# Kernel optimization log

Hardware: AMD Instinct MI355X
Metric: run time of the kernel (lower is better)

The kernel has to match this reference:

```python
import jax, jax.numpy as jnp
import numpy as np

B, C_IN, C_OUT, H, W = 32, 256, 256, 32, 32


def setup_inputs() -> dict:
    key = jax.random.key(0)
    kx, kw, kb = jax.random.split(key, 3)
    x = jax.random.normal(kx, (B, C_IN, H, W), dtype=jnp.float32)
    # 1x1 conv == pointwise linear over channels: weight [out_c, in_c], bias [out_c]
    conv_w = jax.random.normal(kw, (C_OUT, C_IN), dtype=jnp.float32) * (1.0 / np.sqrt(C_IN))
    conv_b = jax.random.normal(kb, (C_OUT,), dtype=jnp.float32) * 0.01
    return {"x": x, "conv_w": conv_w, "conv_b": conv_b}


def reference(x, conv_w, conv_b):
    b, c, h, w = x.shape
    hw = h * w
    q = x.reshape(b, c, hw)  # q == k == flattened x
    # score[b,i,j] = sum_c q[b,c,i] * q[b,c,j]  -> (b, hw, hw)
    score = jnp.einsum('bci,bcj->bij', q, q)
    attn = jax.nn.softmax(score, axis=-1)
    # 1x1 conv V projection: (b, out_c, h, w)
    v = jnp.einsum('oc,bchw->bohw', conv_w, x) + conv_b[None, :, None, None]
    v = v.reshape(b, -1, hw).transpose(0, 2, 1)  # (b, hw, out_c)
    out = jnp.einsum('bij,bjo->bio', attn, v)  # (b, hw, out_c)
    # torch does .transpose(-1,-1) (a no-op) then reshape(b,-1,h,w) in row-major
    out = out.reshape(b, -1, h, w)  # (b, out_c, h, w), position-major flatten as in torch
    # MaxPool2d(2): 2x2 windows, stride 2
    oc = out.shape[1]
    out = out.reshape(b, oc, h // 2, 2, w // 2, 2).max(axis=(3, 5))
    return out
```

## Files before the change

### kernel.cpp

```cpp
#include <hip/hip_runtime.h>
#include <math.h>

#define BB 32
#define CC 256
#define NN 1024
#define THR 8.0f

typedef unsigned short u16;
typedef unsigned int u32;
typedef u16 u16x8 __attribute__((ext_vector_type(8)));
typedef _Float16 h16;
typedef h16 h16x2 __attribute__((ext_vector_type(2)));
typedef h16 h16x8 __attribute__((ext_vector_type(8)));
typedef float f32x4 __attribute__((ext_vector_type(4)));
typedef float f32x16 __attribute__((ext_vector_type(16)));
typedef u32 u32x4v __attribute__((ext_vector_type(4)));

__device__ __forceinline__ h16x8 ldh8(const u16* p) {
    return __builtin_bit_cast(h16x8, *(const u16x8*)p);
}
__device__ __forceinline__ f32x4 mfma16(h16x8 a, h16x8 b, f32x4 c) {
    return __builtin_amdgcn_mfma_f32_16x16x32_f16(a, b, c, 0, 0, 0);
}
__device__ __forceinline__ f32x16 mfma32(h16x8 a, h16x8 b, f32x16 c) {
    return __builtin_amdgcn_mfma_f32_32x32x16_f16(a, b, c, 0, 0, 0);
}
__device__ __forceinline__ void gll16(const void* g, void* l) {
    __builtin_amdgcn_global_load_lds((const __attribute__((address_space(1))) u32*)g,
                                     (__attribute__((address_space(3))) u32*)l, 16, 0, 0);
}

__global__ __launch_bounds__(256) void k_split(const float* __restrict__ x,
                                               u16* __restrict__ qf,
                                               const float* __restrict__ w,
                                               u16* __restrict__ whf) {
    __shared__ float lds[64][65];
    int bid = blockIdx.x;
    int t = threadIdx.x;
    if (bid >= 2048) {
        int s = (bid - 2048) * 256 + t;
        int ot = s >> 9, ks = (s >> 6) & 7, l = s & 63;
        const float* src = w + (size_t)(ot * 16 + (l & 15)) * CC + ks * 32 + 8 * (l >> 4);
        float4 a = *(const float4*)src;
        float4 c = *(const float4*)(src + 4);
        u16x8 o;
        o[0] = __builtin_bit_cast(u16, (h16)a.x); o[1] = __builtin_bit_cast(u16, (h16)a.y);
        o[2] = __builtin_bit_cast(u16, (h16)a.z); o[3] = __builtin_bit_cast(u16, (h16)a.w);
        o[4] = __builtin_bit_cast(u16, (h16)c.x); o[5] = __builtin_bit_cast(u16, (h16)c.y);
        o[6] = __builtin_bit_cast(u16, (h16)c.z); o[7] = __builtin_bit_cast(u16, (h16)c.w);
        *(u16x8*)(whf + (size_t)s * 8) = o;
        return;
    }
    int b = bid >> 6, ct = (bid >> 4) & 3, pt = bid & 15;
    int c0 = ct * 64, p0 = pt * 64;
    const float* xb = x + ((size_t)b * CC + c0) * NN + p0;
#pragma unroll
    for (int it = 0; it < 4; ++it) {
        int cl = (t >> 4) + it * 16;
        int pl = (t & 15) * 4;
        float4 v = *(const float4*)(xb + (size_t)cl * NN + pl);
        lds[pl + 0][cl] = v.x;
        lds[pl + 1][cl] = v.y;
        lds[pl + 2][cl] = v.z;
        lds[pl + 3][cl] = v.w;
    }
    __syncthreads();
    u16* qb = qf + ((size_t)b * NN + p0) * CC + c0;
#pragma unroll
    for (int it = 0; it < 2; ++it) {
        int pl = (t >> 3) + it * 32;
        int cl = (t & 7) * 8;
        u16x8 hv;
#pragma unroll
        for (int e = 0; e < 8; ++e) hv[e] = __builtin_bit_cast(u16, (h16)lds[pl][cl + e]);
        *(u16x8*)(qb + (size_t)pl * CC + cl) = hv;
    }
}

__global__ __launch_bounds__(256, 4) void k_vgemm(const u16* __restrict__ qf,
                                                  const u16* __restrict__ whf,
                                                  const float* __restrict__ bias,
                                                  u16* __restrict__ vimg) {
    __shared__ __align__(16) u16 smem[10240];
    int bid = blockIdx.x;
    int b = bid >> 5, pt = bid & 31;
    int t = threadIdx.x, wave = t >> 6, lane = t & 63;
    int l15 = lane & 15, l4 = lane >> 4;
    int p0 = pt * 32, o0 = wave * 64;
    {
        int Gb = wave * 256;
#pragma unroll
        for (int inst = 0; inst < 4; ++inst) {
            int G = Gb + inst * 64 + lane;
            int row = G >> 5, g = G & 31;
            gll16(qf + (size_t)(b * NN + p0 + row) * CC + ((g ^ (row & 7)) << 3),
                  smem + (size_t)(Gb + inst * 64) * 8);
        }
    }
    __syncthreads();
    f32x4 acc[4][2];
#pragma unroll
    for (int m = 0; m < 4; ++m)
#pragma unroll
        for (int n = 0; n < 2; ++n) acc[m][n] = (f32x4){0.f, 0.f, 0.f, 0.f};
#pragma unroll
    for (int ks = 0; ks < 8; ++ks) {
        h16x8 afr[4], bfr[2];
#pragma unroll
        for (int m = 0; m < 4; ++m)
            afr[m] = ldh8(whf + (size_t)(((wave * 4 + m) * 8 + ks) * 64 + lane) * 8);
#pragma unroll
        for (int n = 0; n < 2; ++n) {
            int row = n * 16 + l15;
            bfr[n] = ldh8(smem + row * 256 + (((4 * ks + l4) ^ (l15 & 7)) << 3));
        }
#pragma unroll
        for (int m = 0; m < 4; ++m)
#pragma unroll
            for (int n = 0; n < 2; ++n) acc[m][n] = mfma16(afr[m], bfr[n], acc[m][n]);
    }
    __syncthreads();
    u16* Vs = smem + wave * 2560;
#pragma unroll
    for (int m = 0; m < 4; ++m) {
#pragma unroll
        for (int r = 0; r < 4; ++r) {
            int ol = m * 16 + 4 * l4 + r;
            float bv = bias[o0 + ol];
#pragma unroll
            for (int n = 0; n < 2; ++n)
                Vs[ol * 40 + n * 16 + l15] =
                    __builtin_bit_cast(u16, (h16)(acc[m][n][r] + bv));
        }
    }
#pragma unroll
    for (int m = 0; m < 4; ++m) {
        u16x8 v = *(u16x8*)&Vs[(m * 16 + l15) * 40 + 8 * l4];
        *(u16x8*)(vimg + ((size_t)(b * 32 + pt) * 256 + o0 + m * 16 + l15) * 32 + 8 * l4) = v;
    }
}

#define SMEM_A 66560
__global__ __launch_bounds__(256, 2) void k_attn(const u16* __restrict__ qf,
                                                 const u16* __restrict__ vimg,
                                                 float* __restrict__ out) {
    __shared__ __align__(16) char smem[SMEM_A];
    u16* Kb = (u16*)smem;
    u16* Vb = (u16*)(smem + 32768);
    float* Mx = (float*)(smem + 65536);
    float* Lx = (float*)(smem + 66048);
    float* Ob = (float*)smem;

    int bid = blockIdx.x;
    int xcd = bid & 7, s0 = bid >> 3;
    int b = xcd * 4 + (s0 >> 4);
    int i0 = (s0 & 15) * 64;
    int t = threadIdx.x, wave = t >> 6, lane = t & 63;
    int rg = wave & 1, jg = wave >> 1;
    int l31 = lane & 31, lh = lane >> 5, l7 = lane & 7;
    const u16* qb = qf + (size_t)b * NN * CC;
    const u16* vtb = vimg + (size_t)b * (32 * 8192);

    {
        int Gb = wave * 512;
#pragma unroll
        for (int inst = 0; inst < 8; ++inst) {
            int G = Gb + inst * 64 + lane;
            int row = (G >> 5) & 31, g = G & 31, tile = G >> 10;
            gll16(qb + (size_t)(i0 + tile * 32 + row) * CC + ((g ^ (row & 7)) << 3),
                  Kb + (size_t)(Gb + inst * 64) * 8);
        }
    }
    __syncthreads();
    h16x8 qfr[16];
    {
        const u16* qB = Kb + rg * 8192 + l31 * 256;
#pragma unroll
        for (int ks = 0; ks < 16; ++ks)
            qfr[ks] = ldh8(qB + (((2 * ks + lh) ^ l7) << 3));
    }
    __syncthreads();
    {
        int Gb = wave * 512;
#pragma unroll
        for (int inst = 0; inst < 8; ++inst) {
            int G = Gb + inst * 64 + lane;
            int row = (G >> 5) & 31, g = G & 31, tile = G >> 10;
            gll16(qb + (size_t)((tile * 16) * 32 + row) * CC + ((g ^ (row & 7)) << 3),
                  Kb + (size_t)(Gb + inst * 64) * 8);
        }
#pragma unroll
        for (int inst = 0; inst < 8; ++inst) {
            int G = Gb + inst * 64 + lane;
            int row = (G >> 2) & 255, gi = G & 3, tile = G >> 10;
            gll16(vtb + (size_t)(tile * 16) * 8192 + row * 32 + ((gi ^ ((row >> 1) & 3)) << 3),
                  Vb + (size_t)(Gb + inst * 64) * 8);
        }
    }
    __syncthreads();

    f32x16 oacc[8];
#pragma unroll
    for (int oc = 0; oc < 8; ++oc)
#pragma unroll
        for (int r = 0; r < 16; ++r) oacc[oc][r] = 0.f;
    float m = -INFINITY, l = 0.f;
    const u16* KbJ = Kb + jg * 8192;
    const u16* VbJ = Vb + jg * 8192;
    int l31s = (l31 >> 1) & 3;

    for (int it = 0; it < 16; ++it) {
        f32x16 s;
#pragma unroll
        for (int r = 0; r < 16; ++r) s[r] = 0.f;
        __builtin_amdgcn_s_setprio(1);
#pragma unroll
        for (int ks = 0; ks < 16; ++ks) {
            h16x8 a = ldh8(KbJ + l31 * 256 + (((2 * ks + lh) ^ l7) << 3));
            s = mfma32(a, qfr[ks], s);
        }
        __builtin_amdgcn_s_setprio(0);
        __syncthreads();
        if (it < 15) {
            int Gb = wave * 512;
#pragma unroll
            for (int inst = 0; inst < 8; ++inst) {
                int G = Gb + inst * 64 + lane;
                int row = (G >> 5) & 31, g = G & 31, tile = G >> 10;
                gll16(qb + (size_t)((tile * 16 + it + 1) * 32 + row) * CC +
                          ((g ^ (row & 7)) << 3),
                      Kb + (size_t)(Gb + inst * 64) * 8);
            }
        }
        float mx = s[0];
#pragma unroll
        for (int r = 1; r < 16; ++r) mx = fmaxf(mx, s[r]);
        mx = fmaxf(mx, __shfl_xor(mx, 32));
        if (__any(mx > m + THR)) {
            float mn = fmaxf(m, mx);
            float f = __expf(m - mn);
            m = mn;
            l *= f;
#pragma unroll
            for (int oc = 0; oc < 8; ++oc)
#pragma unroll
                for (int r = 0; r < 16; ++r) oacc[oc][r] *= f;
        }
        float p[16], rs = 0.f;
#pragma unroll
        for (int r = 0; r < 16; ++r) { p[r] = __expf(s[r] - m); rs += p[r]; }
        rs += __shfl_xor(rs, 32);
        l += rs;
        u32 pk0 = __builtin_bit_cast(u32, __builtin_amdgcn_cvt_pkrtz(p[0], p[1]));
        u32 pk1 = __builtin_bit_cast(u32, __builtin_amdgcn_cvt_pkrtz(p[2], p[3]));
        u32 pk2 = __builtin_bit_cast(u32, __builtin_amdgcn_cvt_pkrtz(p[4], p[5]));
        u32 pk3 = __builtin_bit_cast(u32, __builtin_amdgcn_cvt_pkrtz(p[6], p[7]));
        u32 pk4 = __builtin_bit_cast(u32, __builtin_amdgcn_cvt_pkrtz(p[8], p[9]));
        u32 pk5 = __builtin_bit_cast(u32, __builtin_amdgcn_cvt_pkrtz(p[10], p[11]));
        u32 pk6 = __builtin_bit_cast(u32, __builtin_amdgcn_cvt_pkrtz(p[12], p[13]));
        u32 pk7 = __builtin_bit_cast(u32, __builtin_amdgcn_cvt_pkrtz(p[14], p[15]));
        asm volatile("v_permlane32_swap_b32 %0, %1" : "+v"(pk0), "+v"(pk2));
        asm volatile("v_permlane32_swap_b32 %0, %1" : "+v"(pk1), "+v"(pk3));
        asm volatile("v_permlane32_swap_b32 %0, %1" : "+v"(pk4), "+v"(pk6));
        asm volatile("v_permlane32_swap_b32 %0, %1" : "+v"(pk5), "+v"(pk7));
        h16x8 pa0 = __builtin_bit_cast(h16x8, (u32x4v){pk0, pk1, pk2, pk3});
        h16x8 pa1 = __builtin_bit_cast(h16x8, (u32x4v){pk4, pk5, pk6, pk7});
        __builtin_amdgcn_s_setprio(1);
#pragma unroll
        for (int oc = 0; oc < 8; ++oc) {
            h16x8 v0 = ldh8(VbJ + (oc * 32 + l31) * 32 + (((0 + lh) ^ l31s) << 3));
            h16x8 v1 = ldh8(VbJ + (oc * 32 + l31) * 32 + (((2 + lh) ^ l31s) << 3));
            oacc[oc] = mfma32(v0, pa0, oacc[oc]);
            oacc[oc] = mfma32(v1, pa1, oacc[oc]);
        }
        __builtin_amdgcn_s_setprio(0);
        __syncthreads();
        if (it < 15) {
            int Gb = wave * 512;
#pragma unroll
            for (int inst = 0; inst < 8; ++inst) {
                int G = Gb + inst * 64 + lane;
                int row = (G >> 2) & 255, gi = G & 3, tile = G >> 10;
                gll16(vtb + (size_t)(tile * 16 + it + 1) * 8192 + row * 32 +
                          ((gi ^ ((row >> 1) & 3)) << 3),
                      Vb + (size_t)(Gb + inst * 64) * 8);
            }
        }
    }

    if (lane < 32) {
        Mx[wave * 32 + l31] = m;
        Lx[wave * 32 + l31] = l;
    }
    if (jg == 1) {
#pragma unroll
        for (int oc = 0; oc < 8; ++oc)
#pragma unroll
            for (int q = 0; q < 4; ++q) {
                f32x4 v = (f32x4){oacc[oc][4 * q + 0], oacc[oc][4 * q + 1],
                                  oacc[oc][4 * q + 2], oacc[oc][4 * q + 3]};
                *(f32x4*)&Ob[(((rg * 8 + oc) * 4 + q) * 64 + lane) * 4] = v;
            }
    }
    __syncthreads();
    if (jg == 0) {
        int pidx = (wave ^ 2) * 32 + l31;
        float m2 = Mx[pidx], l2 = Lx[pidx];
        float ms = fmaxf(m, m2);
        float f0 = __expf(m - ms), f1 = __expf(m2 - ms);
        float inv = 1.f / (l * f0 + l2 * f1);
        f0 *= inv; f1 *= inv;
#pragma unroll
        for (int oc = 0; oc < 8; ++oc)
#pragma unroll
            for (int q = 0; q < 4; ++q) {
                f32x4 o1 = *(const f32x4*)&Ob[(((rg * 8 + oc) * 4 + q) * 64 + lane) * 4];
#pragma unroll
                for (int e = 0; e < 4; ++e)
                    oacc[oc][4 * q + e] = oacc[oc][4 * q + e] * f0 + o1[e] * f1;
            }
        int I = i0 + rg * 32 + l31;
        float* ob = out + ((size_t)(b * 256 + (I >> 2)) * 16 + (I & 3) * 4) * 16;
#pragma unroll
        for (int pl = 0; pl < 4; ++pl) {
#pragma unroll
            for (int pwh = 0; pwh < 8; ++pwh) {
                int r0 = 2 * (pwh & 1) + 4 * (pwh >> 1);
                int oc0 = 2 * pl;
                float v = fmaxf(fmaxf(oacc[oc0][r0], oacc[oc0][r0 + 1]),
                                fmaxf(oacc[oc0 + 1][r0], oacc[oc0 + 1][r0 + 1]));
                int pw = (pwh & 1) + 4 * (pwh >> 1) + 2 * lh;
                ob[pl * 16 + pw] = v;
            }
        }
    }
}

extern "C" void kernel_launch(void* const* d_in, const int* in_sizes, int n_in,
                              void* d_out, int out_size, void* d_ws, size_t ws_size,
                              hipStream_t stream) {
    const float* x = (const float*)d_in[0];
    const float* w = (const float*)d_in[1];
    const float* bias = (const float*)d_in[2];
    float* out = (float*)d_out;
    u16* qf = (u16*)d_ws;
    u16* vimg = qf + (size_t)BB * NN * CC;
    u16* whf = vimg + (size_t)BB * NN * CC;
    k_split<<<2080, 256, 0, stream>>>(x, qf, w, whf);
    k_vgemm<<<1024, 256, 0, stream>>>(qf, whf, bias, vimg);
    k_attn<<<512, 256, 0, stream>>>(qf, vimg, out);
}
```

Before: 172.9 us.

## Fuse x conversion into V-GEMM and store K/V in MFMA fragment order

Merges the fp32-to-fp16 transpose pass into the V projection kernel, which now converts x through LDS and writes both K and V straight into MFMA fragment layouts. The attention kernel then loads Q fragments directly from global memory, double-buffers only K in LDS, and streams V fragments from global into registers without staging. The max-pool output is gathered in LDS so stores are coalesced. This removes one full pass over x and the swizzled LDS staging, at the cost of uncached global V loads inside the inner loop.

```diff
diff --git a/kernel.cpp b/kernel.cpp
--- a/kernel.cpp
+++ b/kernel.cpp
@@ -10,7 +10,6 @@
 typedef unsigned int u32;
 typedef u16 u16x8 __attribute__((ext_vector_type(8)));
 typedef _Float16 h16;
-typedef h16 h16x2 __attribute__((ext_vector_type(2)));
 typedef h16 h16x8 __attribute__((ext_vector_type(8)));
 typedef float f32x4 __attribute__((ext_vector_type(4)));
 typedef float f32x16 __attribute__((ext_vector_type(16)));
@@ -25,131 +24,120 @@
 __device__ __forceinline__ f32x16 mfma32(h16x8 a, h16x8 b, f32x16 c) {
     return __builtin_amdgcn_mfma_f32_32x32x16_f16(a, b, c, 0, 0, 0);
 }
+__device__ __forceinline__ u32 pkrtz(float a, float b) {
+    return __builtin_bit_cast(u32, __builtin_amdgcn_cvt_pkrtz(a, b));
+}
 __device__ __forceinline__ void gll16(const void* g, void* l) {
     __builtin_amdgcn_global_load_lds((const __attribute__((address_space(1))) u32*)g,
                                      (__attribute__((address_space(3))) u32*)l, 16, 0, 0);
 }
 
-__global__ __launch_bounds__(256) void k_split(const float* __restrict__ x,
-                                               u16* __restrict__ qf,
-                                               const float* __restrict__ w,
+__global__ __launch_bounds__(256) void k_wprep(const float* __restrict__ w,
                                                u16* __restrict__ whf) {
-    __shared__ float lds[64][65];
-    int bid = blockIdx.x;
-    int t = threadIdx.x;
-    if (bid >= 2048) {
-        int s = (bid - 2048) * 256 + t;
-        int ot = s >> 9, ks = (s >> 6) & 7, l = s & 63;
-        const float* src = w + (size_t)(ot * 16 + (l & 15)) * CC + ks * 32 + 8 * (l >> 4);
-        float4 a = *(const float4*)src;
-        float4 c = *(const float4*)(src + 4);
-        u16x8 o;
-        o[0] = __builtin_bit_cast(u16, (h16)a.x); o[1] = __builtin_bit_cast(u16, (h16)a.y);
-        o[2] = __builtin_bit_cast(u16, (h16)a.z); o[3] = __builtin_bit_cast(u16, (h16)a.w);
-        o[4] = __builtin_bit_cast(u16, (h16)c.x); o[5] = __builtin_bit_cast(u16, (h16)c.y);
-        o[6] = __builtin_bit_cast(u16, (h16)c.z); o[7] = __builtin_bit_cast(u16, (h16)c.w);
-        *(u16x8*)(whf + (size_t)s * 8) = o;
-        return;
-    }
-    int b = bid >> 6, ct = (bid >> 4) & 3, pt = bid & 15;
-    int c0 = ct * 64, p0 = pt * 64;
-    const float* xb = x + ((size_t)b * CC + c0) * NN + p0;
-#pragma unroll
-    for (int it = 0; it < 4; ++it) {
-        int cl = (t >> 4) + it * 16;
-        int pl = (t & 15) * 4;
-        float4 v = *(const float4*)(xb + (size_t)cl * NN + pl);
-        lds[pl + 0][cl] = v.x;
-        lds[pl + 1][cl] = v.y;
-        lds[pl + 2][cl] = v.z;
-        lds[pl + 3][cl] = v.w;
-    }
-    __syncthreads();
-    u16* qb = qf + ((size_t)b * NN + p0) * CC + c0;
-#pragma unroll
-    for (int it = 0; it < 2; ++it) {
-        int pl = (t >> 3) + it * 32;
-        int cl = (t & 7) * 8;
-        u16x8 hv;
-#pragma unroll
-        for (int e = 0; e < 8; ++e) hv[e] = __builtin_bit_cast(u16, (h16)lds[pl][cl + e]);
-        *(u16x8*)(qb + (size_t)pl * CC + cl) = hv;
-    }
-}
-
-__global__ __launch_bounds__(256, 4) void k_vgemm(const u16* __restrict__ qf,
+    int s = blockIdx.x * 256 + threadIdx.x;
+    int ot = s >> 9, ks = (s >> 6) & 7, l = s & 63;
+    const float* src = w + (size_t)(ot * 16 + (l & 15)) * CC + ks * 32 + 8 * (l >> 4);
+    float4 a = *(const float4*)src;
+    float4 c = *(const float4*)(src + 4);
+    u32x4v o = (u32x4v){pkrtz(a.x, a.y), pkrtz(a.z, a.w), pkrtz(c.x, c.y), pkrtz(c.z, c.w)};
+    *(u32x4v*)(whf + (size_t)s * 8) = o;
+}
+
+__global__ __launch_bounds__(256, 4) void k_xform(const float* __restrict__ x,
                                                   const u16* __restrict__ whf,
                                                   const float* __restrict__ bias,
-                                                  u16* __restrict__ vimg) {
-    __shared__ __align__(16) u16 smem[10240];
+                                                  u16* __restrict__ kf,
+                                                  u16* __restrict__ vf) {
+    __shared__ __align__(16) float xs[32][68];
+    __shared__ __align__(16) u16 Vs[4][64 * 40];
     int bid = blockIdx.x;
     int b = bid >> 5, pt = bid & 31;
     int t = threadIdx.x, wave = t >> 6, lane = t & 63;
-    int l15 = lane & 15, l4 = lane >> 4;
-    int p0 = pt * 32, o0 = wave * 64;
-    {
-        int Gb = wave * 256;
-#pragma unroll
-        for (int inst = 0; inst < 4; ++inst) {
-            int G = Gb + inst * 64 + lane;
-            int row = G >> 5, g = G & 31;
-            gll16(qf + (size_t)(b * NN + p0 + row) * CC + ((g ^ (row & 7)) << 3),
-                  smem + (size_t)(Gb + inst * 64) * 8);
-        }
-    }
-    __syncthreads();
+    int l15 = lane & 15, l4 = lane >> 4, l31 = lane & 31, lh = lane >> 5;
+    int p0 = pt * 32;
+    int r0 = t >> 3, pq = (t & 7) * 4;
+
     f32x4 acc[4][2];
 #pragma unroll
     for (int m = 0; m < 4; ++m)
 #pragma unroll
         for (int n = 0; n < 2; ++n) acc[m][n] = (f32x4){0.f, 0.f, 0.f, 0.f};
-#pragma unroll
-    for (int ks = 0; ks < 8; ++ks) {
-        h16x8 afr[4], bfr[2];
-#pragma unroll
-        for (int m = 0; m < 4; ++m)
-            afr[m] = ldh8(whf + (size_t)(((wave * 4 + m) * 8 + ks) * 64 + lane) * 8);
-#pragma unroll
-        for (int n = 0; n < 2; ++n) {
-            int row = n * 16 + l15;
-            bfr[n] = ldh8(smem + row * 256 + (((4 * ks + l4) ^ (l15 & 7)) << 3));
-        }
-#pragma unroll
-        for (int m = 0; m < 4; ++m)
-#pragma unroll
-            for (int n = 0; n < 2; ++n) acc[m][n] = mfma16(afr[m], bfr[n], acc[m][n]);
-    }
-    __syncthreads();
-    u16* Vs = smem + wave * 2560;
+
+    float4 lv0 = *(const float4*)(x + (size_t)(b * CC + r0) * NN + p0 + pq);
+    float4 lv1 = *(const float4*)(x + (size_t)(b * CC + 32 + r0) * NN + p0 + pq);
+
+    for (int cc = 0; cc < 4; ++cc) {
+        xs[pq + 0][r0] = lv0.x; xs[pq + 1][r0] = lv0.y;
+        xs[pq + 2][r0] = lv0.z; xs[pq + 3][r0] = lv0.w;
+        xs[pq + 0][r0 + 32] = lv1.x; xs[pq + 1][r0 + 32] = lv1.y;
+        xs[pq + 2][r0 + 32] = lv1.z; xs[pq + 3][r0 + 32] = lv1.w;
+        __syncthreads();
+        if (cc < 3) {
+            lv0 = *(const float4*)(x + (size_t)(b * CC + (cc + 1) * 64 + r0) * NN + p0 + pq);
+            lv1 = *(const float4*)(x + (size_t)(b * CC + (cc + 1) * 64 + 32 + r0) * NN + p0 + pq);
+        }
+        {
+            const float* sp = &xs[l31][wave * 16 + 8 * lh];
+            f32x4 a = *(const f32x4*)sp;
+            f32x4 c2 = *(const f32x4*)(sp + 4);
+            u32x4v o = (u32x4v){pkrtz(a[0], a[1]), pkrtz(a[2], a[3]),
+                                pkrtz(c2[0], c2[1]), pkrtz(c2[2], c2[3])};
+            *(u32x4v*)(kf + ((size_t)((b * 32 + pt) * 16 + cc * 4 + wave) * 64 + lane) * 8) = o;
+        }
+#pragma unroll
+        for (int ksl = 0; ksl < 2; ++ksl) {
+            int ks = cc * 2 + ksl;
+            h16x8 afr[4], bfr[2];
+#pragma unroll
+            for (int m = 0; m < 4; ++m)
+                afr[m] = ldh8(whf + (size_t)(((wave * 4 + m) * 8 + ks) * 64 + lane) * 8);
+#pragma unroll
+            for (int n = 0; n < 2; ++n) {
+                const float* sp = &xs[n * 16 + l15][ksl * 32 + 8 * l4];
+                f32x4 w0 = *(const f32x4*)sp;
+                f32x4 w1 = *(const f32x4*)(sp + 4);
+                u32x4v tv = (u32x4v){pkrtz(w0[0], w0[1]), pkrtz(w0[2], w0[3]),
+                                     pkrtz(w1[0], w1[1]), pkrtz(w1[2], w1[3])};
+                bfr[n] = __builtin_bit_cast(h16x8, tv);
+            }
+#pragma unroll
+            for (int m = 0; m < 4; ++m)
+#pragma unroll
+                for (int n = 0; n < 2; ++n) acc[m][n] = mfma16(afr[m], bfr[n], acc[m][n]);
+        }
+        __syncthreads();
+    }
+
+    u16* Vsw = &Vs[wave][0];
 #pragma unroll
     for (int m = 0; m < 4; ++m) {
 #pragma unroll
         for (int r = 0; r < 4; ++r) {
             int ol = m * 16 + 4 * l4 + r;
-            float bv = bias[o0 + ol];
+            float bv = bias[wave * 64 + ol];
 #pragma unroll
             for (int n = 0; n < 2; ++n)
-                Vs[ol * 40 + n * 16 + l15] =
+                Vsw[ol * 40 + n * 16 + l15] =
                     __builtin_bit_cast(u16, (h16)(acc[m][n][r] + bv));
         }
     }
 #pragma unroll
-    for (int m = 0; m < 4; ++m) {
-        u16x8 v = *(u16x8*)&Vs[(m * 16 + l15) * 40 + 8 * l4];
-        *(u16x8*)(vimg + ((size_t)(b * 32 + pt) * 256 + o0 + m * 16 + l15) * 32 + 8 * l4) = v;
-    }
-}
-
-#define SMEM_A 66560
-__global__ __launch_bounds__(256, 2) void k_attn(const u16* __restrict__ qf,
-                                                 const u16* __restrict__ vimg,
+    for (int ocs = 0; ocs < 2; ++ocs) {
+#pragma unroll
+        for (int ksl = 0; ksl < 2; ++ksl) {
+            u16x8 v = *(u16x8*)&Vsw[(ocs * 32 + l31) * 40 + ksl * 16 + 8 * lh];
+            *(u16x8*)(vf + ((((size_t)(b * 32 + pt) * 8 + wave * 2 + ocs) * 2 + ksl) * 64 +
+                            lane) * 8) = v;
+        }
+    }
+}
+
+__global__ __launch_bounds__(256, 2) void k_attn(const u16* __restrict__ kf,
+                                                 const u16* __restrict__ vf,
                                                  float* __restrict__ out) {
-    __shared__ __align__(16) char smem[SMEM_A];
-    u16* Kb = (u16*)smem;
-    u16* Vb = (u16*)(smem + 32768);
+    __shared__ __align__(16) char smem[66560];
     float* Mx = (float*)(smem + 65536);
     float* Lx = (float*)(smem + 66048);
-    float* Ob = (float*)smem;
 
     int bid = blockIdx.x;
     int xcd = bid & 7, s0 = bid >> 3;
@@ -157,47 +145,27 @@
     int i0 = (s0 & 15) * 64;
     int t = threadIdx.x, wave = t >> 6, lane = t & 63;
     int rg = wave & 1, jg = wave >> 1;
-    int l31 = lane & 31, lh = lane >> 5, l7 = lane & 7;
-    const u16* qb = qf + (size_t)b * NN * CC;
-    const u16* vtb = vimg + (size_t)b * (32 * 8192);
-
-    {
-        int Gb = wave * 512;
-#pragma unroll
-        for (int inst = 0; inst < 8; ++inst) {
-            int G = Gb + inst * 64 + lane;
-            int row = (G >> 5) & 31, g = G & 31, tile = G >> 10;
-            gll16(qb + (size_t)(i0 + tile * 32 + row) * CC + ((g ^ (row & 7)) << 3),
-                  Kb + (size_t)(Gb + inst * 64) * 8);
-        }
-    }
-    __syncthreads();
+    int l31 = lane & 31, lh = lane >> 5;
+    const u16* kfb = kf + (size_t)b * NN * CC;
+    const u16* vfb = vf + (size_t)b * NN * CC;
+
     h16x8 qfr[16];
     {
-        const u16* qB = Kb + rg * 8192 + l31 * 256;
+        int itq = (i0 >> 5) + rg;
 #pragma unroll
         for (int ks = 0; ks < 16; ++ks)
-            qfr[ks] = ldh8(qB + (((2 * ks + lh) ^ l7) << 3));
-    }
-    __syncthreads();
+            qfr[ks] = ldh8(kfb + ((size_t)(itq * 16 + ks) * 64 + lane) * 8);
+    }
+
     {
-        int Gb = wave * 512;
+        int tile = jg * 16;
 #pragma unroll
         for (int inst = 0; inst < 8; ++inst) {
-            int G = Gb + inst * 64 + lane;
-            int row = (G >> 5) & 31, g = G & 31, tile = G >> 10;
-            gll16(qb + (size_t)((tile * 16) * 32 + row) * CC + ((g ^ (row & 7)) << 3),
-                  Kb + (size_t)(Gb + inst * 64) * 8);
-        }
-#pragma unroll
-        for (int inst = 0; inst < 8; ++inst) {
-            int G = Gb + inst * 64 + lane;
-            int row = (G >> 2) & 255, gi = G & 3, tile = G >> 10;
-            gll16(vtb + (size_t)(tile * 16) * 8192 + row * 32 + ((gi ^ ((row >> 1) & 3)) << 3),
-                  Vb + (size_t)(Gb + inst * 64) * 8);
-        }
-    }
-    __syncthreads();
+            int sl = rg * 8 + inst;
+            gll16(kfb + ((size_t)(tile * 16 + sl) * 64 + lane) * 8,
+                  smem + jg * 32768 + sl * 1024);
+        }
+    }
 
     f32x16 oacc[8];
 #pragma unroll
@@ -205,33 +173,32 @@
 #pragma unroll
         for (int r = 0; r < 16; ++r) oacc[oc][r] = 0.f;
     float m = -INFINITY, l = 0.f;
-    const u16* KbJ = Kb + jg * 8192;
-    const u16* VbJ = Vb + jg * 8192;
-    int l31s = (l31 >> 1) & 3;
+    __syncthreads();
 
     for (int it = 0; it < 16; ++it) {
+        int cur = it & 1;
+        int jt = jg * 16 + it;
+        const u16* KbC = (const u16*)(smem + jg * 32768 + cur * 16384);
+        if (it < 15) {
+            int tile = jt + 1;
+#pragma unroll
+            for (int inst = 0; inst < 8; ++inst) {
+                int sl = rg * 8 + inst;
+                gll16(kfb + ((size_t)(tile * 16 + sl) * 64 + lane) * 8,
+                      smem + jg * 32768 + (cur ^ 1) * 16384 + sl * 1024);
+            }
+        }
         f32x16 s;
 #pragma unroll
         for (int r = 0; r < 16; ++r) s[r] = 0.f;
         __builtin_amdgcn_s_setprio(1);
 #pragma unroll
         for (int ks = 0; ks < 16; ++ks) {
-            h16x8 a = ldh8(KbJ + l31 * 256 + (((2 * ks + lh) ^ l7) << 3));
+            h16x8 a = ldh8(KbC + (ks * 64 + lane) * 8);
             s = mfma32(a, qfr[ks], s);
         }
         __builtin_amdgcn_s_setprio(0);
-        __syncthreads();
-        if (it < 15) {
-            int Gb = wave * 512;
-#pragma unroll
-            for (int inst = 0; inst < 8; ++inst) {
-                int G = Gb + inst * 64 + lane;
-                int row = (G >> 5) & 31, g = G & 31, tile = G >> 10;
-                gll16(qb + (size_t)((tile * 16 + it + 1) * 32 + row) * CC +
-                          ((g ^ (row & 7)) << 3),
-                      Kb + (size_t)(Gb + inst * 64) * 8);
-            }
-        }
+
         float mx = s[0];
 #pragma unroll
         for (int r = 1; r < 16; ++r) mx = fmaxf(mx, s[r]);
@@ -251,47 +218,41 @@
         for (int r = 0; r < 16; ++r) { p[r] = __expf(s[r] - m); rs += p[r]; }
         rs += __shfl_xor(rs, 32);
         l += rs;
-        u32 pk0 = __builtin_bit_cast(u32, __builtin_amdgcn_cvt_pkrtz(p[0], p[1]));
-        u32 pk1 = __builtin_bit_cast(u32, __builtin_amdgcn_cvt_pkrtz(p[2], p[3]));
-        u32 pk2 = __builtin_bit_cast(u32, __builtin_amdgcn_cvt_pkrtz(p[4], p[5]));
-        u32 pk3 = __builtin_bit_cast(u32, __builtin_amdgcn_cvt_pkrtz(p[6], p[7]));
-        u32 pk4 = __builtin_bit_cast(u32, __builtin_amdgcn_cvt_pkrtz(p[8], p[9]));
-        u32 pk5 = __builtin_bit_cast(u32, __builtin_amdgcn_cvt_pkrtz(p[10], p[11]));
-        u32 pk6 = __builtin_bit_cast(u32, __builtin_amdgcn_cvt_pkrtz(p[12], p[13]));
-        u32 pk7 = __builtin_bit_cast(u32, __builtin_amdgcn_cvt_pkrtz(p[14], p[15]));
+
+        u32 pk0 = pkrtz(p[0], p[1]), pk1 = pkrtz(p[2], p[3]);
+        u32 pk2 = pkrtz(p[4], p[5]), pk3 = pkrtz(p[6], p[7]);
+        u32 pk4 = pkrtz(p[8], p[9]), pk5 = pkrtz(p[10], p[11]);
+        u32 pk6 = pkrtz(p[12], p[13]), pk7 = pkrtz(p[14], p[15]);
         asm volatile("v_permlane32_swap_b32 %0, %1" : "+v"(pk0), "+v"(pk2));
         asm volatile("v_permlane32_swap_b32 %0, %1" : "+v"(pk1), "+v"(pk3));
         asm volatile("v_permlane32_swap_b32 %0, %1" : "+v"(pk4), "+v"(pk6));
         asm volatile("v_permlane32_swap_b32 %0, %1" : "+v"(pk5), "+v"(pk7));
         h16x8 pa0 = __builtin_bit_cast(h16x8, (u32x4v){pk0, pk1, pk2, pk3});
         h16x8 pa1 = __builtin_bit_cast(h16x8, (u32x4v){pk4, pk5, pk6, pk7});
+
+        const u16* vt = vfb + (size_t)jt * 8192;
+        u16x8 v0n = *(const u16x8*)(vt + lane * 8);
+        u16x8 v1n = *(const u16x8*)(vt + 512 + lane * 8);
         __builtin_amdgcn_s_setprio(1);
 #pragma unroll
         for (int oc = 0; oc < 8; ++oc) {
-            h16x8 v0 = ldh8(VbJ + (oc * 32 + l31) * 32 + (((0 + lh) ^ l31s) << 3));
-            h16x8 v1 = ldh8(VbJ + (oc * 32 + l31) * 32 + (((2 + lh) ^ l31s) << 3));
-            oacc[oc] = mfma32(v0, pa0, oacc[oc]);
-            oacc[oc] = mfma32(v1, pa1, oacc[oc]);
+            u16x8 v0 = v0n, v1 = v1n;
+            if (oc < 7) {
+                v0n = *(const u16x8*)(vt + (size_t)((oc + 1) * 2) * 512 + lane * 8);
+                v1n = *(const u16x8*)(vt + (size_t)((oc + 1) * 2 + 1) * 512 + lane * 8);
+            }
+            oacc[oc] = mfma32(__builtin_bit_cast(h16x8, v0), pa0, oacc[oc]);
+            oacc[oc] = mfma32(__builtin_bit_cast(h16x8, v1), pa1, oacc[oc]);
         }
         __builtin_amdgcn_s_setprio(0);
         __syncthreads();
-        if (it < 15) {
-            int Gb = wave * 512;
-#pragma unroll
-            for (int inst = 0; inst < 8; ++inst) {
-                int G = Gb + inst * 64 + lane;
-                int row = (G >> 2) & 255, gi = G & 3, tile = G >> 10;
-                gll16(vtb + (size_t)(tile * 16 + it + 1) * 8192 + row * 32 +
-                          ((gi ^ ((row >> 1) & 3)) << 3),
-                      Vb + (size_t)(Gb + inst * 64) * 8);
-            }
-        }
     }
 
     if (lane < 32) {
         Mx[wave * 32 + l31] = m;
         Lx[wave * 32 + l31] = l;
     }
+    float* Ob = (float*)smem;
     if (jg == 1) {
 #pragma unroll
         for (int oc = 0; oc < 8; ++oc)
@@ -319,19 +280,31 @@
                 for (int e = 0; e < 4; ++e)
                     oacc[oc][4 * q + e] = oacc[oc][4 * q + e] * f0 + o1[e] * f1;
             }
-        int I = i0 + rg * 32 + l31;
-        float* ob = out + ((size_t)(b * 256 + (I >> 2)) * 16 + (I & 3) * 4) * 16;
-#pragma unroll
-        for (int pl = 0; pl < 4; ++pl) {
-#pragma unroll
-            for (int pwh = 0; pwh < 8; ++pwh) {
-                int r0 = 2 * (pwh & 1) + 4 * (pwh >> 1);
-                int oc0 = 2 * pl;
-                float v = fmaxf(fmaxf(oacc[oc0][r0], oacc[oc0][r0 + 1]),
-                                fmaxf(oacc[oc0 + 1][r0], oacc[oc0 + 1][r0 + 1]));
-                int pw = (pwh & 1) + 4 * (pwh >> 1) + 2 * lh;
-                ob[pl * 16 + pw] = v;
-            }
+    }
+    __syncthreads();
+    float* PoolBuf = (float*)smem;
+    if (jg == 0) {
+        int il = rg * 32 + l31;
+#pragma unroll
+        for (int oc2 = 0; oc2 < 4; ++oc2)
+#pragma unroll
+            for (int q = 0; q < 4; ++q)
+#pragma unroll
+                for (int b1 = 0; b1 < 2; ++b1) {
+                    int r = 4 * q + 2 * b1;
+                    float v = fmaxf(fmaxf(oacc[2 * oc2][r], oacc[2 * oc2][r + 1]),
+                                    fmaxf(oacc[2 * oc2 + 1][r], oacc[2 * oc2 + 1][r + 1]));
+                    PoolBuf[il * 68 + oc2 * 16 + q * 4 + lh * 2 + b1] = v;
+                }
+    }
+    __syncthreads();
+    {
+        float* ob = out + ((size_t)b * 256 + (i0 >> 2)) * 256;
+        int row = t >> 2, cb = (t & 3) * 16;
+#pragma unroll
+        for (int e = 0; e < 4; ++e) {
+            f32x4 vv = *(f32x4*)&PoolBuf[row * 68 + cb + e * 4];
+            *(f32x4*)&ob[row * 64 + cb + e * 4] = vv;
         }
     }
 }
@@ -343,10 +316,10 @@
     const float* w = (const float*)d_in[1];
     const float* bias = (const float*)d_in[2];
     float* out = (float*)d_out;
-    u16* qf = (u16*)d_ws;
-    u16* vimg = qf + (size_t)BB * NN * CC;
-    u16* whf = vimg + (size_t)BB * NN * CC;
-    k_split<<<2080, 256, 0, stream>>>(x, qf, w, whf);
-    k_vgemm<<<1024, 256, 0, stream>>>(qf, whf, bias, vimg);
-    k_attn<<<512, 256, 0, stream>>>(qf, vimg, out);
-}
+    u16* kf = (u16*)d_ws;
+    u16* vf = kf + (size_t)BB * NN * CC;
+    u16* whf = vf + (size_t)BB * NN * CC;
+    k_wprep<<<32, 256, 0, stream>>>(w, whf);
+    k_xform<<<1024, 256, 0, stream>>>(x, whf, bias, kf, vf);
+    k_attn<<<512, 256, 0, stream>>>(kf, vf, out);
+}
```

New measurement: 144.7 us. -16.3%, faster.
